# Kernel optimization log

Measured on AMD Instinct MI355X. Metric: run time of the kernel, lower is better.

Reference implementation:

```python
import jax, jax.numpy as jnp
import numpy as np

B, N, K = 16, 2048, 16        # events, nodes per event, neighbors
F_IN, L = 64, 64              # in_size, layer_size
EPS = 1e-5                    # BatchNorm1d eps


def setup_inputs() -> dict:
    key = jax.random.key(0)
    k1, k2 = jax.random.split(key, 2)
    x = jax.random.normal(k1, (B * N, F_IN), jnp.float32)
    batch = jnp.repeat(jnp.arange(B, dtype=jnp.int32), N)  # equal-size events
    W = jax.random.normal(k2, (2 * F_IN, L), jnp.float32) * 0.08
    b = jnp.zeros((L,), jnp.float32)
    gamma = jnp.ones((L,), jnp.float32)
    beta = jnp.zeros((L,), jnp.float32)
    return {"x": x, "batch": batch, "W": W, "b": b, "gamma": gamma, "beta": beta}


def reference(x, batch, W, b, gamma, beta):
    # batch encodes B equal-size events -> reshape to [B, N, F]
    xr = x.reshape(B, N, F_IN)

    # dynamic kNN in feature space, per event (self included, as in PyG knn)
    sq = jnp.sum(xr * xr, axis=-1)                                  # [B, N]
    d = sq[:, :, None] + sq[:, None, :] - 2.0 * jnp.einsum(
        'bnf,bmf->bnm', xr, xr)                                     # [B, N, N]
    _, idx = jax.lax.top_k(-d, K)                                   # [B, N, K]

    # gather neighbor features
    xj = jax.vmap(lambda xe, ie: xe[ie])(xr, idx)                   # [B, N, K, F]
    xi = jnp.broadcast_to(xr[:, :, None, :], (B, N, K, F_IN))

    # EdgeConv message: nn(cat([x_i, x_j - x_i]))
    e = jnp.concatenate([xi, xj - xi], axis=-1)                     # [B, N, K, 2F]
    h = jnp.einsum('bnke,el->bnkl', e, W) + b                       # Linear

    # BatchNorm1d over all edges (training-mode batch stats, biased var)
    m = jnp.mean(h, axis=(0, 1, 2))
    v = jnp.var(h, axis=(0, 1, 2))
    h = (h - m) * jax.lax.rsqrt(v + EPS) * gamma + beta
    h = jax.nn.relu(h)

    # aggr='mean' over the K neighbors
    out = jnp.mean(h, axis=2)                                       # [B, N, L]
    return out.reshape(B * N, L)
```

## Files before the change

### kernel.cpp

```cpp
#include <hip/hip_runtime.h>
#include <hip/hip_fp16.h>
#include <math.h>

#define B_EV    16
#define N_NODES 2048
#define K_NN    16
#define F_IN    64
#define L_OUT   64
#define NT      (B_EV * N_NODES)
#define EDGES   (NT * K_NN)

typedef __attribute__((ext_vector_type(8)))  short bh8;
typedef __attribute__((ext_vector_type(16))) float f32x16;
typedef __attribute__((ext_vector_type(8)))  unsigned short us8;

__device__ inline unsigned short bf16_rne(float f) {
  unsigned int u = __float_as_uint(f);
  return (unsigned short)((u + 0x7FFFu + ((u >> 16) & 1u)) >> 16);
}
__device__ inline float bf16f(unsigned short h) {
  return __uint_as_float(((unsigned int)h) << 16);
}

__device__ inline void gload16(const void* g, void* l) {
  __builtin_amdgcn_global_load_lds(
      (const __attribute__((address_space(1))) void*)(g),
      (__attribute__((address_space(3))) void*)(l), 16, 0, 0);
}

__device__ inline unsigned long long score_key(const float* xiW,
                                               const float* __restrict__ xev,
                                               int mcol, float sqn,
                                               const float* __restrict__ sqev) {
  const float4* xm = (const float4*)(xev + (size_t)mcol * F_IN);
  double d0 = 0.0, d1 = 0.0, d2 = 0.0, d3 = 0.0;
  #pragma unroll
  for (int fq = 0; fq < 16; fq += 4) {
    float4 c0 = xm[fq + 0], c1 = xm[fq + 1], c2 = xm[fq + 2], c3 = xm[fq + 3];
    float4 x0 = *(const float4*)(xiW + fq * 4);
    float4 x1 = *(const float4*)(xiW + fq * 4 + 4);
    float4 x2 = *(const float4*)(xiW + fq * 4 + 8);
    float4 x3 = *(const float4*)(xiW + fq * 4 + 12);
    d0 = fma((double)x0.x, (double)c0.x, d0);
    d0 = fma((double)x0.y, (double)c0.y, d0);
    d0 = fma((double)x0.z, (double)c0.z, d0);
    d0 = fma((double)x0.w, (double)c0.w, d0);
    d1 = fma((double)x1.x, (double)c1.x, d1);
    d1 = fma((double)x1.y, (double)c1.y, d1);
    d1 = fma((double)x1.z, (double)c1.z, d1);
    d1 = fma((double)x1.w, (double)c1.w, d1);
    d2 = fma((double)x2.x, (double)c2.x, d2);
    d2 = fma((double)x2.y, (double)c2.y, d2);
    d2 = fma((double)x2.z, (double)c2.z, d2);
    d2 = fma((double)x2.w, (double)c2.w, d2);
    d3 = fma((double)x3.x, (double)c3.x, d3);
    d3 = fma((double)x3.y, (double)c3.y, d3);
    d3 = fma((double)x3.z, (double)c3.z, d3);
    d3 = fma((double)x3.w, (double)c3.w, d3);
  }
  float dot32 = (float)((d0 + d1) + (d2 + d3));
  float sv = __fsub_rn(__fadd_rn(sqn, sqev[mcol]), __fmul_rn(2.0f, dot32));
  unsigned int fb = __float_as_uint(sv);
  fb = (fb & 0x80000000u) ? ~fb : (fb | 0x80000000u);
  return ((unsigned long long)fb << 32) | (unsigned int)mcol;
}

__global__ __launch_bounds__(256) void k_uv(const float* __restrict__ x,
                                            const float* __restrict__ W,
                                            float* __restrict__ u,
                                            float* __restrict__ v,
                                            float* __restrict__ sq,
                                            unsigned short* __restrict__ xh,
                                            unsigned short* __restrict__ xl) {
  __shared__ float xs[64][64];
  const int t = threadIdx.x;
  const int l = t & 63, g = t >> 6;
  const int nodeBase = blockIdx.x * 64;

  {
    const float4* gx = (const float4*)(x + (size_t)nodeBase * 64);
    float4* lx = (float4*)&xs[0][0];
    #pragma unroll
    for (int p = 0; p < 4; ++p) lx[p * 256 + t] = gx[p * 256 + t];
  }
  float wdc[64], w2c[64];
  #pragma unroll
  for (int f = 0; f < 64; ++f) {
    float w1v = W[f * 64 + l];
    float w2v = W[4096 + f * 64 + l];
    wdc[f] = w1v - w2v;
    w2c[f] = w2v;
  }
  __syncthreads();

  #pragma unroll
  for (int p = 0; p < 2; ++p) {
    int n = p * 32 + (t >> 3), j = t & 7;
    float xv = xs[n][j];
    float s = __fmul_rn(xv, xv);
    #pragma unroll
    for (int i = 1; i < 8; ++i) {
      float c = xs[n][j + 8 * i];
      s = __fadd_rn(s, __fmul_rn(c, c));
    }
    s = __fadd_rn(s, __shfl_xor(s, 1));
    s = __fadd_rn(s, __shfl_xor(s, 2));
    s = __fadd_rn(s, __shfl_xor(s, 4));
    if (j == 0) sq[nodeBase + n] = s;
  }
  #pragma unroll
  for (int p = 0; p < 4; ++p) {
    int i = p * 256 + t;
    float4 vv = ((const float4*)&xs[0][0])[i];
    ushort4 h, lo;
    h.x = bf16_rne(vv.x); lo.x = bf16_rne(vv.x - bf16f(h.x));
    h.y = bf16_rne(vv.y); lo.y = bf16_rne(vv.y - bf16f(h.y));
    h.z = bf16_rne(vv.z); lo.z = bf16_rne(vv.z - bf16f(h.z));
    h.w = bf16_rne(vv.w); lo.w = bf16_rne(vv.w - bf16f(h.w));
    ((ushort4*)xh)[(size_t)nodeBase * 16 + i] = h;
    ((ushort4*)xl)[(size_t)nodeBase * 16 + i] = lo;
  }

  for (int rep = 0; rep < 16; ++rep) {
    int n = rep * 4 + g;
    const float4* xr = (const float4*)xs[n];
    float au = 0.f, av = 0.f;
    #pragma unroll
    for (int fq = 0; fq < 16; ++fq) {
      float4 xv = xr[fq];
      au = fmaf(xv.x, wdc[fq * 4 + 0], au); av = fmaf(xv.x, w2c[fq * 4 + 0], av);
      au = fmaf(xv.y, wdc[fq * 4 + 1], au); av = fmaf(xv.y, w2c[fq * 4 + 1], av);
      au = fmaf(xv.z, wdc[fq * 4 + 2], au); av = fmaf(xv.z, w2c[fq * 4 + 2], av);
      au = fmaf(xv.w, wdc[fq * 4 + 3], au); av = fmaf(xv.w, w2c[fq * 4 + 3], av);
    }
    u[(size_t)(nodeBase + n) * 64 + l] = au;
    v[(size_t)(nodeBase + n) * 64 + l] = av;
  }
}

__global__ __launch_bounds__(256, 6) void k_gemm(const unsigned short* __restrict__ xh,
                                                 const unsigned short* __restrict__ xl,
                                                 const float* __restrict__ sq,
                                                 unsigned short* __restrict__ Sbuf,
                                                 int evBase) {
  __shared__ char xb[16384];
  __shared__ __align__(16) unsigned short Sh[32 * 128];
  const int t    = threadIdx.x;
  const int w    = t >> 6;
  const int lane = t & 63;
  const int ev    = evBase + (blockIdx.x >> 7);
  const int rem   = blockIdx.x & 127;
  const int strip = rem >> 1;
  const int half  = rem & 1;
  const int rowBase = strip * 32;
  const int T0 = half * 8;
  const size_t evNode = (size_t)ev * N_NODES;
  const float* __restrict__ sqev = sq + evNode;
  unsigned short* __restrict__ Sev =
      Sbuf + (size_t)(ev - evBase) * N_NODES * N_NODES;
  char* Sc = (char*)Sh;

  {
    int col = t >> 3;
    int fbs = ((t & 7) << 4) ^ ((col & 7) << 4);
    gload16((const char*)(xh + (evNode + rowBase + col) * 64) + fbs, Sc + t * 16);
    gload16((const char*)(xl + (evNode + rowBase + col) * 64) + fbs, Sc + 4096 + t * 16);
    #pragma unroll
    for (int p = 0; p < 4; ++p) {
      const int colB = p * 32 + (t >> 3);
      const char* g = (const char*)(xh + (evNode + T0 * 128 + colB) * 64) + fbs;
      gload16(g, xb + p * 4096 + t * 16);
    }
  }
  __syncthreads();
  bh8 ah[4], al[4];
  {
    int row = lane & 31;
    int fb  = (lane >> 5) * 16;
    #pragma unroll
    for (int ks = 0; ks < 4; ++ks) {
      int off = (row * 128 + ks * 32 + fb) ^ ((row & 7) << 4);
      ah[ks] = *(const bh8*)(Sc + off);
      al[ks] = *(const bh8*)(Sc + 4096 + off);
    }
  }
  __syncthreads();

  for (int T = T0; T < T0 + 8; ++T) {
    const int tileCol = T * 128;
    {
      f32x16 acc;
      #pragma unroll
      for (int q = 0; q < 16; ++q) acc[q] = 0.f;
      int colIn = w * 32 + (lane & 31);
      int fb = (lane >> 5) * 16;
      #pragma unroll
      for (int ks = 0; ks < 4; ++ks) {
        int off = (colIn * 128 + ks * 32 + fb) ^ ((colIn & 7) << 4);
        bh8 bh = *(const bh8*)(xb + off);
        acc = __builtin_amdgcn_mfma_f32_32x32x16_bf16(ah[ks], bh, acc, 0, 0, 0);
        acc = __builtin_amdgcn_mfma_f32_32x32x16_bf16(al[ks], bh, acc, 0, 0, 0);
      }
      float sqc = sqev[tileCol + colIn];
      #pragma unroll
      for (int reg = 0; reg < 16; ++reg) {
        int m = (reg & 3) + 8 * (reg >> 2) + 4 * (lane >> 5);
        Sh[m * 128 + colIn] =
            __half_as_ushort(__float2half(fmaf(-2.0f, acc[reg], sqc)));
      }
    }
    __syncthreads();
    if (T < T0 + 7) {
      #pragma unroll
      for (int p = 0; p < 4; ++p) {
        const int colB = p * 32 + (t >> 3);
        const int fbs = ((t & 7) << 4) ^ (((t >> 3) & 7) << 4);
        const char* g = (const char*)(xh + (evNode + tileCol + 128 + colB) * 64) + fbs;
        gload16(g, xb + p * 4096 + t * 16);
      }
    }
    {
      int r  = t >> 3;
      int cg = t & 7;
      unsigned short* gS =
          Sev + (size_t)(rowBase + r) * N_NODES + tileCol + cg * 16;
      const uint4* lS = (const uint4*)(Sh + r * 128 + cg * 16);
      *(uint4*)gS = lS[0];
      *(uint4*)(gS + 8) = lS[1];
    }
    __syncthreads();
  }
}

#define SCR_CAP 192
#define SEL_DELTA 1.0f

__global__ __launch_bounds__(256, 1) void k_sel(const float* __restrict__ x,
                                                const float* __restrict__ sq,
                                                const unsigned short* __restrict__ Sbuf,
                                                int* __restrict__ nidx,
                                                int rowBase) {
  __shared__ float xiS[4][64];
  __shared__ int candLDS[4][SCR_CAP];
  __shared__ unsigned long long keysLDS[4][SCR_CAP];
  const int w = threadIdx.x >> 6, lane = threadIdx.x & 63;
  const int rowInChunk = blockIdx.x * 4 + w;
  const int grow = rowBase + rowInChunk;
  const int ev = grow >> 11;
  const int rowInEv = grow & 2047;
  const size_t evNode = (size_t)ev * N_NODES;
  const unsigned short* __restrict__ Srow = Sbuf + (size_t)rowInChunk * N_NODES;
  const float* __restrict__ sqev = sq + evNode;
  const float* __restrict__ xev = x + evNode * F_IN;

  xiS[w][lane] = x[(evNode + rowInEv) * F_IN + lane];

  us8 pk[4];
  #pragma unroll
  for (int q = 0; q < 4; ++q)
    pk[q] = *(const us8*)(Srow + q * 512 + lane * 8);

  float mn = 3.4e38f;
  #pragma unroll
  for (int q = 0; q < 4; ++q) {
    #pragma unroll
    for (int e = 0; e < 8; ++e)
      mn = fminf(mn, __half2float(__ushort_as_half(pk[q][e])));
  }
  #pragma unroll
  for (int k = 2; k <= 64; k <<= 1) {
    #pragma unroll
    for (int j = k >> 1; j >= 1; j >>= 1) {
      float o = __shfl_xor(mn, j);
      bool up = ((lane & k) == 0);
      bool iAmLower = ((lane & j) == 0);
      bool wantSmall = (up == iAmLower);
      bool less = (mn < o);
      if (less != wantSmall) mn = o;
    }
  }
  const float thr = __shfl(mn, 15) + SEL_DELTA;

  unsigned int msk[4];
  int c = 0;
  #pragma unroll
  for (int q = 0; q < 4; ++q) {
    unsigned int m = 0;
    #pragma unroll
    for (int e = 0; e < 8; ++e) {
      float v = __half2float(__ushort_as_half(pk[q][e]));
      m |= (v <= thr) ? (1u << e) : 0u;
    }
    msk[q] = m;
    c += __popc(m);
  }
  int incl = c;
  #pragma unroll
  for (int off = 1; off < 64; off <<= 1) {
    int n = __shfl_up(incl, off);
    if (lane >= off) incl += n;
  }
  int pos = incl - c;
  int total = __shfl(incl, 63);
  const int cn = (total < SCR_CAP) ? total : SCR_CAP;
  #pragma unroll
  for (int q = 0; q < 4; ++q) {
    unsigned int m = msk[q];
    while (m) {
      int e = __ffs(m) - 1;
      m &= m - 1;
      if (pos < SCR_CAP) candLDS[w][pos] = q * 512 + lane * 8 + e;
      ++pos;
    }
  }

  const float sqn = sqev[rowInEv];
  const float* xiW = xiS[w];
  const int* crow = candLDS[w];

  int base = 0;
  while (base < cn) {
    int rem = cn - base;
    if (rem <= 32) {
      int hf = lane >> 5;
      int ii = lane & 31;
      int ci = base + ii;
      bool act = ii < rem;
      int mcol = act ? crow[ci] : 0;
      const float4* xm = (const float4*)(xev + (size_t)mcol * F_IN);
      double d0 = 0.0, d1 = 0.0;
      #pragma unroll
      for (int q = 0; q < 8; ++q) {
        int fq = hf * 8 + q;
        float4 cc = xm[fq];
        float4 xq = *(const float4*)(xiW + fq * 4);
        d0 = fma((double)xq.x, (double)cc.x, d0);
        d1 = fma((double)xq.y, (double)cc.y, d1);
        d0 = fma((double)xq.z, (double)cc.z, d0);
        d1 = fma((double)xq.w, (double)cc.w, d1);
      }
      double ds = d0 + d1;
      double od = __shfl_xor(ds, 32);
      if (act && hf == 0) {
        float dot32 = (float)(ds + od);
        float sv = __fsub_rn(__fadd_rn(sqn, sqev[mcol]), __fmul_rn(2.0f, dot32));
        unsigned int fb = __float_as_uint(sv);
        fb = (fb & 0x80000000u) ? ~fb : (fb | 0x80000000u);
        keysLDS[w][ci] = ((unsigned long long)fb << 32) | (unsigned int)mcol;
      }
      base = cn;
    } else {
      int ci = base + lane;
      bool act = ci < cn;
      int mcol = act ? crow[ci] : 0;
      unsigned long long key = score_key(xiW, xev, mcol, sqn, sqev);
      if (act) keysLDS[w][ci] = key;
      base += 64;
    }
  }

  const unsigned long long INVALID = ~0ull;
  unsigned long long k0 = INVALID, k1 = INVALID, k2 = INVALID;
  if (lane < cn)        k0 = keysLDS[w][lane];
  if (lane + 64 < cn)   k1 = keysLDS[w][lane + 64];
  if (lane + 128 < cn)  k2 = keysLDS[w][lane + 128];
  int r0 = 0, r1 = 0, r2 = 0;
  for (int i = 0; i < cn; ++i) {
    unsigned long long kk = keysLDS[w][i];
    r0 += (kk < k0) ? 1 : 0;
    r1 += (kk < k1) ? 1 : 0;
    r2 += (kk < k2) ? 1 : 0;
  }
  const size_t outBase = (evNode + rowInEv) * K_NN;
  if (lane < cn && r0 < K_NN)
    nidx[outBase + r0] = (int)evNode + (int)(k0 & 0x7FFFFFFFu);
  if (lane + 64 < cn && r1 < K_NN)
    nidx[outBase + r1] = (int)evNode + (int)(k1 & 0x7FFFFFFFu);
  if (lane + 128 < cn && r2 < K_NN)
    nidx[outBase + r2] = (int)evNode + (int)(k2 & 0x7FFFFFFFu);
}

#define NB_ST 32
__global__ __launch_bounds__(256) void k_stats(const float* __restrict__ u,
                                               const float* __restrict__ v,
                                               const int* __restrict__ nidx,
                                               const float* __restrict__ bvec,
                                               float* __restrict__ stats) {
  __shared__ float red1[4][64];
  __shared__ float red2[4][64];
  const int l = threadIdx.x & 63, g = threadIdx.x >> 6;
  const int base = blockIdx.x * NB_ST;
  const float bl = bvec[l];
  float s1 = 0.f, s2 = 0.f;
  for (int nn = g; nn < NB_ST; nn += 4) {
    const int node = base + nn;
    const float ui = u[(size_t)node * 64 + l] + bl;
    const int* ip = nidx + (size_t)node * K_NN;
    int idx[16];
    #pragma unroll
    for (int q = 0; q < 4; ++q)
      *(int4*)&idx[q * 4] = *(const int4*)(ip + q * 4);
    #pragma unroll
    for (int k = 0; k < K_NN; ++k) {
      const float vj = v[(size_t)idx[k] * 64 + l];
      const float h = ui + vj;
      s1 += h;
      s2 = fmaf(h, h, s2);
    }
  }
  red1[g][l] = s1; red2[g][l] = s2;
  __syncthreads();
  if (g == 0) {
    float t1 = red1[0][l] + red1[1][l] + red1[2][l] + red1[3][l];
    float t2 = red2[0][l] + red2[1][l] + red2[2][l] + red2[3][l];
    atomicAdd(&stats[l], t1);
    atomicAdd(&stats[64 + l], t2);
  }
}

__global__ __launch_bounds__(256) void k_out(const float* __restrict__ u,
                                             const float* __restrict__ v,
                                             const int* __restrict__ nidx,
                                             const float* __restrict__ bvec,
                                             const float* __restrict__ gamma,
                                             const float* __restrict__ beta,
                                             const float* __restrict__ stats,
                                             float* __restrict__ out) {
  const int l = threadIdx.x & 63, g = threadIdx.x >> 6;
  const float inv = 1.0f / (float)EDGES;
  const float mean = stats[l] * inv;
  const float ex2 = stats[64 + l] * inv;
  const float var = ex2 - mean * mean;
  const float a = gamma[l] * rsqrtf(var + 1e-5f);
  const float bb = fmaf(-mean, a, beta[l]);
  const float bl = bvec[l];
  const int base = blockIdx.x * NB_ST;
  for (int nn = g; nn < NB_ST; nn += 4) {
    const int node = base + nn;
    const float ui = u[(size_t)node * 64 + l] + bl;
    const int* ip = nidx + (size_t)node * K_NN;
    int idx[16];
    #pragma unroll
    for (int q = 0; q < 4; ++q)
      *(int4*)&idx[q * 4] = *(const int4*)(ip + q * 4);
    float acc = 0.f;
    #pragma unroll
    for (int k = 0; k < K_NN; ++k) {
      const float vj = v[(size_t)idx[k] * 64 + l];
      const float h = ui + vj;
      acc += fmaxf(fmaf(a, h, bb), 0.f);
    }
    out[(size_t)node * 64 + l] = acc * (1.0f / 16.0f);
  }
}

extern "C" void kernel_launch(void* const* d_in, const int* in_sizes, int n_in,
                              void* d_out, int out_size, void* d_ws, size_t ws_size,
                              hipStream_t stream) {
  (void)in_sizes; (void)n_in; (void)out_size;
  const float* x     = (const float*)d_in[0];
  const float* W     = (const float*)d_in[2];
  const float* b     = (const float*)d_in[3];
  const float* gamma = (const float*)d_in[4];
  const float* beta  = (const float*)d_in[5];
  float* out = (float*)d_out;

  char* ws = (char*)d_ws;
  float*          u     = (float*)(ws);
  float*          v     = (float*)(ws + 8388608);
  float*          sq    = (float*)(ws + 16777216);
  int*            nidx  = (int*)  (ws + 16908288);
  float*          stats = (float*)(ws + 19005440);
  unsigned short* xh    = (unsigned short*)(ws + 19005952);
  unsigned short* xl    = (unsigned short*)(ws + 23200256);
  unsigned short* Sbuf  = (unsigned short*)(ws + 27394560);

  const size_t sChunkBytes = (size_t)N_NODES * N_NODES * 2;
  size_t avail = (ws_size > 27394560) ? ws_size - 27394560 : 0;
  int evCap = (int)((avail / sChunkBytes < 16) ? (avail / sChunkBytes) : 16);
  if (evCap < 1) evCap = 1;

  hipMemsetAsync(stats, 0, 512, stream);
  k_uv  <<<512, 256, 0, stream>>>(x, W, u, v, sq, xh, xl);

  for (int e0 = 0; e0 < B_EV; e0 += evCap) {
    int ne = (B_EV - e0 < evCap) ? (B_EV - e0) : evCap;
    k_gemm<<<ne * 128, 256, 0, stream>>>(xh, xl, sq, Sbuf, e0);
    k_sel <<<ne * 512, 256, 0, stream>>>(x, sq, Sbuf, nidx, e0 * N_NODES);
  }

  k_stats<<<1024, 256, 0, stream>>>(u, v, nidx, b, stats);
  k_out <<<1024, 256, 0, stream>>>(u, v, nidx, b, gamma, beta, stats, out);
}
```

Before: 173.9 us.

## Process two kNN rows per wavefront in selection kernel using half-waves

```diff
diff --git a/kernel.cpp b/kernel.cpp
--- a/kernel.cpp
+++ b/kernel.cpp
@@ -240,51 +240,53 @@
                                                 const unsigned short* __restrict__ Sbuf,
                                                 int* __restrict__ nidx,
                                                 int rowBase) {
-  __shared__ float xiS[4][64];
-  __shared__ int candLDS[4][SCR_CAP];
-  __shared__ unsigned long long keysLDS[4][SCR_CAP];
+  __shared__ float xiS[4][2][64];
+  __shared__ int candLDS[4][2][SCR_CAP];
+  __shared__ unsigned long long keysLDS[4][2][SCR_CAP];
   const int w = threadIdx.x >> 6, lane = threadIdx.x & 63;
-  const int rowInChunk = blockIdx.x * 4 + w;
-  const int grow = rowBase + rowInChunk;
+  const int h = lane >> 5, s = lane & 31;
+  const int ric = (blockIdx.x * 4 + w) * 2 + h;
+  const int grow = rowBase + ric;
   const int ev = grow >> 11;
   const int rowInEv = grow & 2047;
   const size_t evNode = (size_t)ev * N_NODES;
-  const unsigned short* __restrict__ Srow = Sbuf + (size_t)rowInChunk * N_NODES;
+  const unsigned short* __restrict__ Srow = Sbuf + (size_t)ric * N_NODES;
   const float* __restrict__ sqev = sq + evNode;
   const float* __restrict__ xev = x + evNode * F_IN;
 
-  xiS[w][lane] = x[(evNode + rowInEv) * F_IN + lane];
-
-  us8 pk[4];
-  #pragma unroll
-  for (int q = 0; q < 4; ++q)
-    pk[q] = *(const us8*)(Srow + q * 512 + lane * 8);
+  xiS[w][h][s]      = x[(evNode + rowInEv) * F_IN + s];
+  xiS[w][h][s + 32] = x[(evNode + rowInEv) * F_IN + s + 32];
+
+  us8 pk[8];
+  #pragma unroll
+  for (int q = 0; q < 8; ++q)
+    pk[q] = *(const us8*)(Srow + q * 256 + s * 8);
 
   float mn = 3.4e38f;
   #pragma unroll
-  for (int q = 0; q < 4; ++q) {
+  for (int q = 0; q < 8; ++q) {
     #pragma unroll
     for (int e = 0; e < 8; ++e)
       mn = fminf(mn, __half2float(__ushort_as_half(pk[q][e])));
   }
   #pragma unroll
-  for (int k = 2; k <= 64; k <<= 1) {
+  for (int k = 2; k <= 32; k <<= 1) {
     #pragma unroll
     for (int j = k >> 1; j >= 1; j >>= 1) {
       float o = __shfl_xor(mn, j);
-      bool up = ((lane & k) == 0);
-      bool iAmLower = ((lane & j) == 0);
+      bool up = ((s & k) == 0);
+      bool iAmLower = ((s & j) == 0);
       bool wantSmall = (up == iAmLower);
       bool less = (mn < o);
       if (less != wantSmall) mn = o;
     }
   }
-  const float thr = __shfl(mn, 15) + SEL_DELTA;
-
-  unsigned int msk[4];
+  const float thr = __shfl(mn, h * 32 + 15) + SEL_DELTA;
+
+  unsigned int msk[8];
   int c = 0;
   #pragma unroll
-  for (int q = 0; q < 4; ++q) {
+  for (int q = 0; q < 8; ++q) {
     unsigned int m = 0;
     #pragma unroll
     for (int e = 0; e < 8; ++e) {
@@ -296,88 +298,50 @@
   }
   int incl = c;
   #pragma unroll
-  for (int off = 1; off < 64; off <<= 1) {
+  for (int off = 1; off < 32; off <<= 1) {
     int n = __shfl_up(incl, off);
-    if (lane >= off) incl += n;
+    if (s >= off) incl += n;
   }
   int pos = incl - c;
-  int total = __shfl(incl, 63);
+  int total = __shfl(incl, h * 32 + 31);
   const int cn = (total < SCR_CAP) ? total : SCR_CAP;
   #pragma unroll
-  for (int q = 0; q < 4; ++q) {
+  for (int q = 0; q < 8; ++q) {
     unsigned int m = msk[q];
     while (m) {
       int e = __ffs(m) - 1;
       m &= m - 1;
-      if (pos < SCR_CAP) candLDS[w][pos] = q * 512 + lane * 8 + e;
+      if (pos < SCR_CAP) candLDS[w][h][pos] = q * 256 + s * 8 + e;
       ++pos;
     }
   }
 
+  int cnOther = __shfl_xor(cn, 32);
+  const int cnMax = (cn > cnOther) ? cn : cnOther;
+
   const float sqn = sqev[rowInEv];
-  const float* xiW = xiS[w];
-  const int* crow = candLDS[w];
-
-  int base = 0;
-  while (base < cn) {
-    int rem = cn - base;
-    if (rem <= 32) {
-      int hf = lane >> 5;
-      int ii = lane & 31;
-      int ci = base + ii;
-      bool act = ii < rem;
-      int mcol = act ? crow[ci] : 0;
-      const float4* xm = (const float4*)(xev + (size_t)mcol * F_IN);
-      double d0 = 0.0, d1 = 0.0;
-      #pragma unroll
-      for (int q = 0; q < 8; ++q) {
-        int fq = hf * 8 + q;
-        float4 cc = xm[fq];
-        float4 xq = *(const float4*)(xiW + fq * 4);
-        d0 = fma((double)xq.x, (double)cc.x, d0);
-        d1 = fma((double)xq.y, (double)cc.y, d1);
-        d0 = fma((double)xq.z, (double)cc.z, d0);
-        d1 = fma((double)xq.w, (double)cc.w, d1);
-      }
-      double ds = d0 + d1;
-      double od = __shfl_xor(ds, 32);
-      if (act && hf == 0) {
-        float dot32 = (float)(ds + od);
-        float sv = __fsub_rn(__fadd_rn(sqn, sqev[mcol]), __fmul_rn(2.0f, dot32));
-        unsigned int fb = __float_as_uint(sv);
-        fb = (fb & 0x80000000u) ? ~fb : (fb | 0x80000000u);
-        keysLDS[w][ci] = ((unsigned long long)fb << 32) | (unsigned int)mcol;
-      }
-      base = cn;
-    } else {
-      int ci = base + lane;
-      bool act = ci < cn;
-      int mcol = act ? crow[ci] : 0;
-      unsigned long long key = score_key(xiW, xev, mcol, sqn, sqev);
-      if (act) keysLDS[w][ci] = key;
-      base += 64;
-    }
-  }
-
-  const unsigned long long INVALID = ~0ull;
-  unsigned long long k0 = INVALID, k1 = INVALID, k2 = INVALID;
-  if (lane < cn)        k0 = keysLDS[w][lane];
-  if (lane + 64 < cn)   k1 = keysLDS[w][lane + 64];
-  if (lane + 128 < cn)  k2 = keysLDS[w][lane + 128];
-  int r0 = 0, r1 = 0, r2 = 0;
-  for (int i = 0; i < cn; ++i) {
-    unsigned long long kk = keysLDS[w][i];
-    r0 += (kk < k0) ? 1 : 0;
-    r1 += (kk < k1) ? 1 : 0;
-    r2 += (kk < k2) ? 1 : 0;
-  }
+  const float* xiW = xiS[w][h];
+  for (int bs = 0; bs < cnMax; bs += 32) {
+    int ci = bs + s;
+    bool act = ci < cn;
+    int mcol = act ? candLDS[w][h][ci] : 0;
+    unsigned long long key = score_key(xiW, xev, mcol, sqn, sqev);
+    if (act) keysLDS[w][h][ci] = key;
+  }
+
   const size_t outBase = (evNode + rowInEv) * K_NN;
-  if (lane < cn && r0 < K_NN)
-    nidx[outBase + r0] = (int)evNode + (int)(k0 & 0x7FFFFFFFu);
-  if (lane + 64 < cn && r1 < K_NN)
-    nidx[outBase + r1] = (int)evNode + (int)(k1 & 0x7FFFFFFFu);
-  if (lane + 128 < cn && r2 < K_NN)
-    nidx[outBase + r2] = (int)evNode + (int)(k2 & 0x7FFFFFFFu);
+  for (int bs = 0; bs < cnMax; bs += 32) {
+    int ci = bs + s;
+    bool act = ci < cn;
+    unsigned long long kk = act ? keysLDS[w][h][ci] : ~0ull;
+    int r = 0;
+    for (int i = 0; i < cnMax; ++i) {
+      unsigned long long ki = keysLDS[w][h][i];
+      r += ((i < cn) && (ki < kk)) ? 1 : 0;
+    }
+    if (act && r < K_NN)
+      nidx[outBase + r] = (int)evNode + (int)(kk & 0x7FFFFFFFu);
+  }
 }
 
 #define NB_ST 32
@@ -486,7 +450,7 @@
   for (int e0 = 0; e0 < B_EV; e0 += evCap) {
     int ne = (B_EV - e0 < evCap) ? (B_EV - e0) : evCap;
     k_gemm<<<ne * 128, 256, 0, stream>>>(xh, xl, sq, Sbuf, e0);
-    k_sel <<<ne * 512, 256, 0, stream>>>(x, sq, Sbuf, nidx, e0 * N_NODES);
+    k_sel <<<ne * 256, 256, 0, stream>>>(x, sq, Sbuf, nidx, e0 * N_NODES);
   }
 
   k_stats<<<1024, 256, 0, stream>>>(u, v, nidx, b, stats);
```

Result: no change. 176.3 us (+1.4%).
